# Performance work log

Measured on AMD Instinct MI355X. Metric: run time of the kernel, lower is better.

## Reference

```python
import jax, jax.numpy as jnp
import numpy as np

B, NV, NT = 256, 64, 77
UNIT_DIM, PROJ_DIM, V_HID, T_HID = 512, 512, 768, 512
TEMP_INIT = 0.07
LN_EPS = 1e-5
NORM_EPS = 1e-12


def _xavier(key, fan_in, fan_out):
    lim = np.sqrt(6.0 / (fan_in + fan_out))
    return jax.random.uniform(key, (fan_in, fan_out), jnp.float32, -lim, lim)


def _ln(x, g, b):
    mu = jnp.mean(x, axis=-1, keepdims=True)
    var = jnp.mean(jnp.square(x - mu), axis=-1, keepdims=True)
    return (x - mu) * jax.lax.rsqrt(var + LN_EPS) * g + b


def _l2norm(x):
    n = jnp.sqrt(jnp.sum(jnp.square(x), axis=-1, keepdims=True))
    return x / jnp.maximum(n, NORM_EPS)


def _unit_mlp(x, W1, b1, g, bt, W2, b2):
    # Linear -> LayerNorm -> GELU(exact) -> Linear
    h = x @ W1 + b1
    h = jax.nn.gelu(_ln(h, g, bt), approximate=False)
    return h @ W2 + b2


def setup_inputs() -> dict:
    key = jax.random.key(0)
    ks = jax.random.split(key, 12)
    inp = {
        'visual_units': jax.random.normal(ks[0], (B, NV, UNIT_DIM), jnp.float32),
        'text_units': jax.random.normal(ks[1], (B, NT, UNIT_DIM), jnp.float32),
        'visual_cls': jax.random.normal(ks[2], (B, V_HID), jnp.float32),
        'text_cls': jax.random.normal(ks[3], (B, T_HID), jnp.float32),
        # visual unit proj
        'vW1': _xavier(ks[4], UNIT_DIM, PROJ_DIM), 'vb1': jnp.zeros(PROJ_DIM),
        'vg': jnp.ones(PROJ_DIM), 'vbt': jnp.zeros(PROJ_DIM),
        'vW2': _xavier(ks[5], PROJ_DIM, PROJ_DIM), 'vb2': jnp.zeros(PROJ_DIM),
        # text unit proj
        'tW1': _xavier(ks[6], UNIT_DIM, PROJ_DIM), 'tb1': jnp.zeros(PROJ_DIM),
        'tg': jnp.ones(PROJ_DIM), 'tbt': jnp.zeros(PROJ_DIM),
        'tW2': _xavier(ks[7], PROJ_DIM, PROJ_DIM), 'tb2': jnp.zeros(PROJ_DIM),
        # global projections (Linear -> LayerNorm)
        'gvW': _xavier(ks[8], V_HID, PROJ_DIM), 'gvb': jnp.zeros(PROJ_DIM),
        'gvg': jnp.ones(PROJ_DIM), 'gvbt': jnp.zeros(PROJ_DIM),
        'gtW': _xavier(ks[9], T_HID, PROJ_DIM), 'gtb': jnp.zeros(PROJ_DIM),
        'gtg': jnp.ones(PROJ_DIM), 'gtbt': jnp.zeros(PROJ_DIM),
        'logit_scale': jnp.log(jnp.asarray(1.0 / TEMP_INIT, jnp.float32)),
    }
    return inp


def _forward(visual_units, text_units, visual_cls, text_cls,
             vW1, vb1, vg, vbt, vW2, vb2,
             tW1, tb1, tg, tbt, tW2, tb2,
             gvW, gvb, gvg, gvbt, gtW, gtb, gtg, gtbt, logit_scale):
    # unit projections, L2-normalized: [B,Nv,P], [B,Nt,P]
    v_proj = _l2norm(_unit_mlp(visual_units, vW1, vb1, vg, vbt, vW2, vb2))
    t_proj = _l2norm(_unit_mlp(text_units, tW1, tb1, tg, tbt, tW2, tb2))
    # global projections, L2-normalized: [B,P]
    v_global = _l2norm(_ln(visual_cls @ gvW + gvb, gvg, gvbt))
    t_global = _l2norm(_ln(text_cls @ gtW + gtb, gtg, gtbt))

    scale = jnp.minimum(jnp.exp(logit_scale), 100.0)

    # ---- global CLIP loss ----
    logits = scale * (v_global @ t_global.T)  # [B,B]
    diag = jnp.arange(B)
    lp_i2t = jax.nn.log_softmax(logits, axis=-1)
    lp_t2i = jax.nn.log_softmax(logits.T, axis=-1)
    loss_global = -(jnp.mean(lp_i2t[diag, diag]) + jnp.mean(lp_t2i[diag, diag])) / 2.0

    # ---- unit-level mutual-NN loss (vectorized version of the python loop) ----
    sim = jnp.einsum('bvp,btp->bvt', v_proj, t_proj) * scale  # [B,Nv,Nt]
    logp_i2t = jax.nn.log_softmax(sim, axis=-1)   # over Nt
    logp_t2i = jax.nn.log_softmax(sim, axis=-2)   # over Nv
    best_t_for_v = jnp.argmax(sim, axis=-1)       # [B,Nv]
    best_v_for_t = jnp.argmax(sim, axis=-2)       # [B,Nt]
    # mutual mask: best_v_for_t[b, best_t_for_v[b,i]] == i
    back = jnp.take_along_axis(best_v_for_t, best_t_for_v, axis=1)  # [B,Nv]
    mutual = (back == jnp.arange(NV)[None, :])                      # [B,Nv] bool
    j = best_t_for_v[..., None]                                     # [B,Nv,1]
    lp1 = jnp.take_along_axis(logp_i2t, j, axis=2)[..., 0]          # [B,Nv]
    lp2 = jnp.take_along_axis(logp_t2i, j, axis=2)[..., 0]          # [B,Nv]
    m = mutual.astype(sim.dtype)
    loss_sum = -jnp.sum(m * (lp1 + lp2))
    count = 2.0 * jnp.sum(m)  # always >= 2B: the per-sample argmax of sim is mutual
    loss_unit = loss_sum / jnp.maximum(count, 1.0)

    # ---- diversity loss ----
    def _diversity(units, n):
        u = _l2norm(units)
        s = jnp.einsum('bip,bjp->bij', u, u)
        mask = 1.0 - jnp.eye(n, dtype=s.dtype)
        return jnp.sum(jnp.abs(s) * mask) / (B * n * (n - 1))
    loss_div = (_diversity(visual_units, NV) + _diversity(text_units, NT)) / 2.0

    sim_matrix = jnp.einsum('bvp,btp->bvt', v_proj, t_proj)
    return loss_global, loss_unit, loss_div, v_proj, t_proj, v_global, t_global, sim_matrix


def reference(visual_units, text_units, visual_cls, text_cls,
              vW1, vb1, vg, vbt, vW2, vb2,
              tW1, tb1, tg, tbt, tW2, tb2,
              gvW, gvb, gvg, gvbt, gtW, gtb, gtg, gtbt, logit_scale):
    return _forward(visual_units, text_units, visual_cls, text_cls,
                    vW1, vb1, vg, vbt, vW2, vb2,
                    tW1, tb1, tg, tbt, tW2, tb2,
                    gvW, gvb, gvg, gvbt, gtW, gtb, gtg, gtbt, logit_scale)
```

## Files before the change

### kernel.cpp

```cpp
#include <hip/hip_runtime.h>
#include <math.h>

typedef __attribute__((ext_vector_type(8))) short short8;
typedef __attribute__((ext_vector_type(4))) short short4v;
typedef __attribute__((ext_vector_type(4))) float f32x4;

#define NB 256
#define NVU 64
#define NTU 77
#define PD 512

#define O_VP 3ull
#define O_TP (O_VP + (size_t)NB * NVU * PD)
#define O_VG (O_TP + (size_t)NB * NTU * PD)
#define O_TG (O_VG + (size_t)NB * PD)
#define O_SM (O_TG + (size_t)NB * PD)

#define WS_VW1T 0u
#define WS_VW2T 524288u
#define WS_TW1T 1048576u
#define WS_TW2T 1572864u
#define WS_GVWT 2097152u
#define WS_GTWT 2883584u
#define WS_LOG  3552256u
#define WS_DIAG 3814400u
#define WS_RLSE 3815424u
#define WS_CLSE 3816448u
#define WS_UP   3817472u
#define WS_UC   3818496u
#define WS_PART 3819520u

#define GL_LDS16(gp, lp) __builtin_amdgcn_global_load_lds( \
    (const __attribute__((address_space(1))) void*)(gp), \
    (__attribute__((address_space(3))) void*)(lp), 16, 0, 0)

__device__ inline short f2bf(float f) {
  union { float f; unsigned u; } v; v.f = f;
  unsigned r = v.u + 0x7FFFu + ((v.u >> 16) & 1u);
  return (short)(r >> 16);
}
__device__ inline float bf2f(short s) {
  union { unsigned u; float f; } v; v.u = ((unsigned)(unsigned short)s) << 16;
  return v.f;
}

__device__ inline float blk_sum_(float x, float* buf, int nw) {
  const int lane = threadIdx.x & 63, w = threadIdx.x >> 6;
  #pragma unroll
  for (int m = 1; m < 64; m <<= 1) x += __shfl_xor(x, m, 64);
  __syncthreads();
  if (lane == 0) buf[w] = x;
  __syncthreads();
  float s = 0.f;
  for (int i = 0; i < nw; ++i) s += buf[i];
  return s;
}
__device__ inline float blk_max_(float x, float* buf, int nw) {
  const int lane = threadIdx.x & 63, w = threadIdx.x >> 6;
  #pragma unroll
  for (int m = 1; m < 64; m <<= 1) x = fmaxf(x, __shfl_xor(x, m, 64));
  __syncthreads();
  if (lane == 0) buf[w] = x;
  __syncthreads();
  float s = buf[0];
  for (int i = 1; i < nw; ++i) s = fmaxf(s, buf[i]);
  return s;
}

__global__ __launch_bounds__(256) void k_cvt_frag4(
    const float* __restrict__ s0, const float* __restrict__ s1,
    const float* __restrict__ s2, const float* __restrict__ s3,
    short* __restrict__ d0, short* __restrict__ d1,
    short* __restrict__ d2, short* __restrict__ d3) {
  int m = blockIdx.x >> 10;
  const float* src = m == 0 ? s0 : m == 1 ? s1 : m == 2 ? s2 : s3;
  short* dst = m == 0 ? d0 : m == 1 ? d1 : m == 2 ? d2 : d3;
  int idx = (blockIdx.x & 1023) * 256 + threadIdx.x;
  int k = idx >> 9, n = idx & 511;
  int kc = k >> 5, t = k & 31;
  int s = t >> 3, j = t & 7;
  int sw = (s ^ ((n >> 1) & 3)) << 3;
  dst[(size_t)kc * 16384 + n * 32 + sw + j] = f2bf(src[idx]);
}

__global__ __launch_bounds__(256) void k_transpose2(
    const float* __restrict__ gv, short* __restrict__ dv_,
    const float* __restrict__ gt, short* __restrict__ dt_) {
  int bid = blockIdx.x;
  if (bid < 1536) {
    int idx = bid * 256 + threadIdx.x;
    int k = idx >> 9, n = idx & 511;
    dv_[(size_t)n * 768 + k] = f2bf(gv[idx]);
  } else {
    int idx = (bid - 1536) * 256 + threadIdx.x;
    int k = idx >> 9, n = idx & 511;
    dt_[(size_t)n * 512 + k] = f2bf(gt[idx]);
  }
}

__global__ __launch_bounds__(1024) void k_unit_mlp11(
    const float* __restrict__ Xv, const float* __restrict__ Xt,
    const short* __restrict__ vWf1, const float* __restrict__ vb1,
    const float* __restrict__ vg, const float* __restrict__ vbt,
    const short* __restrict__ vWf2, const float* __restrict__ vb2,
    const short* __restrict__ tWf1, const float* __restrict__ tb1,
    const float* __restrict__ tg, const float* __restrict__ tbt,
    const short* __restrict__ tWf2, const float* __restrict__ tb2,
    float* __restrict__ outV, float* __restrict__ outT) {
  __shared__ __align__(16) short As[64][520];
  __shared__ __align__(16) short Bs[2][16384];
  __shared__ float redS[4][64];
  __shared__ float redQ[4][64];

  const int tid = threadIdx.x;
  const int w = tid >> 6, lane = tid & 63;
  const int rg = w >> 2, cg = w & 3;
  const int hi = lane >> 4, lo = lane & 15;

  const int xcd = blockIdx.x & 7, ii = blockIdx.x >> 3;
  const int orig = (xcd < 4 ? xcd * 71 : 284 + (xcd - 4) * 70) + ii;
  const bool isv = orig < 256;
  const int rb = isv ? orig : orig - 256;
  const float* __restrict__ X   = isv ? Xv : Xt;
  const short* __restrict__ Wf1 = isv ? vWf1 : tWf1;
  const float* __restrict__ b1  = isv ? vb1  : tb1;
  const float* __restrict__ gg  = isv ? vg   : tg;
  const float* __restrict__ bt  = isv ? vbt  : tbt;
  const short* __restrict__ Wf2 = isv ? vWf2 : tWf2;
  const float* __restrict__ b2  = isv ? vb2  : tb2;
  float* __restrict__ outF      = isv ? outV : outT;
  const size_t row0 = (size_t)rb * 64;

  const int arow = rg * 16 + lo;
  const int bswz = (cg * 128 + lo) * 32 + ((hi ^ ((lo >> 1) & 3)) * 8);

  GL_LDS16(Wf1 + tid * 8, &Bs[0][tid * 8]);
  GL_LDS16(Wf1 + 8192 + tid * 8, &Bs[0][8192 + tid * 8]);

  const f32x4* Xp = (const f32x4*)(X + row0 * 512);
  #pragma unroll
  for (int i = 0; i < 8; ++i) {
    int idx = i * 1024 + tid;
    f32x4 f = __builtin_nontemporal_load(Xp + idx);
    short4v s4 = {f2bf(f[0]), f2bf(f[1]), f2bf(f[2]), f2bf(f[3])};
    *(short4v*)&As[idx >> 7][(idx & 127) * 4] = s4;
  }
  __syncthreads();

  f32x4 acc[8];
  #pragma unroll
  for (int ct = 0; ct < 8; ++ct) acc[ct] = (f32x4){0.f, 0.f, 0.f, 0.f};

  GL_LDS16(Wf1 + 16384 + tid * 8, &Bs[1][tid * 8]);
  GL_LDS16(Wf1 + 16384 + 8192 + tid * 8, &Bs[1][8192 + tid * 8]);

  for (int kc = 0; kc < 16; ++kc) {
    const int cur = kc & 1;
    short8 a = *(const short8*)&As[arow][kc * 32 + hi * 8];
    #pragma unroll
    for (int ct = 0; ct < 8; ++ct) {
      short8 bb = *(const short8*)&Bs[cur][bswz + ct * 512];
      acc[ct] = __builtin_amdgcn_mfma_f32_16x16x32_bf16(a, bb, acc[ct], 0, 0, 0);
    }
    __builtin_amdgcn_s_barrier();
    const int nc = kc + 2;
    const short* nxt = (nc < 16) ? (Wf1 + (size_t)nc * 16384)
                                 : (Wf2 + (size_t)(nc - 16) * 16384);
    GL_LDS16(nxt + tid * 8, &Bs[cur][tid * 8]);
    GL_LDS16(nxt + 8192 + tid * 8, &Bs[cur][8192 + tid * 8]);
    asm volatile("s_waitcnt vmcnt(2)" ::: "memory");
  }

  {
    float ps[4] = {0.f, 0.f, 0.f, 0.f}, pq[4] = {0.f, 0.f, 0.f, 0.f};
    #pragma unroll
    for (int ct = 0; ct < 8; ++ct) {
      float bia = b1[cg * 128 + ct * 16 + lo];
      #pragma unroll
      for (int r = 0; r < 4; ++r) {
        float v = acc[ct][r] + bia;
        acc[ct][r] = v;
        ps[r] += v; pq[r] += v * v;
      }
    }
    #pragma unroll
    for (int m = 1; m < 16; m <<= 1)
      #pragma unroll
      for (int r = 0; r < 4; ++r) {
        ps[r] += __shfl_xor(ps[r], m, 64);
        pq[r] += __shfl_xor(pq[r], m, 64);
      }
    if (lo == 0) {
      #pragma unroll
      for (int r = 0; r < 4; ++r) {
        int rr = rg * 16 + hi * 4 + r;
        redS[cg][rr] = ps[r]; redQ[cg][rr] = pq[r];
      }
    }
  }
  __syncthreads();

  {
    float mu[4], rs[4];
    #pragma unroll
    for (int r = 0; r < 4; ++r) {
      int rr = rg * 16 + hi * 4 + r;
      float s = redS[0][rr] + redS[1][rr] + redS[2][rr] + redS[3][rr];
      float q = redQ[0][rr] + redQ[1][rr] + redQ[2][rr] + redQ[3][rr];
      float m_ = s * (1.f / 512.f);
      mu[r] = m_;
      rs[r] = rsqrtf(q * (1.f / 512.f) - m_ * m_ + 1e-5f);
    }
    #pragma unroll
    for (int ct = 0; ct < 8; ++ct) {
      int col = cg * 128 + ct * 16 + lo;
      float ga = gg[col], be = bt[col];
      #pragma unroll
      for (int r = 0; r < 4; ++r) {
        float xn = (acc[ct][r] - mu[r]) * rs[r] * ga + be;
        float ge = 0.5f * xn * (1.f + erff(xn * 0.70710678118654752f));
        As[rg * 16 + hi * 4 + r][col] = f2bf(ge);
      }
    }
  }
  __syncthreads();

  #pragma unroll
  for (int ct = 0; ct < 8; ++ct) acc[ct] = (f32x4){0.f, 0.f, 0.f, 0.f};
  for (int kc = 0; kc < 16; ++kc) {
    const int cur = kc & 1;
    short8 a = *(const short8*)&As[arow][kc * 32 + hi * 8];
    #pragma unroll
    for (int ct = 0; ct < 8; ++ct) {
      short8 bb = *(const short8*)&Bs[cur][bswz + ct * 512];
      acc[ct] = __builtin_amdgcn_mfma_f32_16x16x32_bf16(a, bb, acc[ct], 0, 0, 0);
    }
    __builtin_amdgcn_s_barrier();
    if (kc < 14) {
      const short* nxt = Wf2 + (size_t)(kc + 2) * 16384;
      GL_LDS16(nxt + tid * 8, &Bs[cur][tid * 8]);
      GL_LDS16(nxt + 8192 + tid * 8, &Bs[cur][8192 + tid * 8]);
      asm volatile("s_waitcnt vmcnt(2)" ::: "memory");
    } else if (kc == 14) {
      asm volatile("s_waitcnt vmcnt(0)" ::: "memory");
    }
  }

  {
    float pq[4] = {0.f, 0.f, 0.f, 0.f};
    #pragma unroll
    for (int ct = 0; ct < 8; ++ct) {
      float bia = b2[cg * 128 + ct * 16 + lo];
      #pragma unroll
      for (int r = 0; r < 4; ++r) {
        float v = acc[ct][r] + bia;
        acc[ct][r] = v;
        pq[r] += v * v;
      }
    }
    #pragma unroll
    for (int m = 1; m < 16; m <<= 1)
      #pragma unroll
      for (int r = 0; r < 4; ++r) pq[r] += __shfl_xor(pq[r], m, 64);
    if (lo == 0) {
      #pragma unroll
      for (int r = 0; r < 4; ++r) redQ[cg][rg * 16 + hi * 4 + r] = pq[r];
    }
  }
  __syncthreads();
  {
    float invn[4];
    #pragma unroll
    for (int r = 0; r < 4; ++r) {
      int rr = rg * 16 + hi * 4 + r;
      float q = redQ[0][rr] + redQ[1][rr] + redQ[2][rr] + redQ[3][rr];
      invn[r] = 1.f / fmaxf(sqrtf(q), 1e-12f);
    }
    #pragma unroll
    for (int ct = 0; ct < 8; ++ct) {
      int col = cg * 128 + ct * 16 + lo;
      #pragma unroll
      for (int r = 0; r < 4; ++r)
        outF[(row0 + rg * 16 + hi * 4 + r) * 512 + col] = acc[ct][r] * invn[r];
    }
  }
}

__global__ __launch_bounds__(256) void k_gproj2(
    const float* __restrict__ vsrc, const float* __restrict__ tsrc,
    const short* __restrict__ vWT, const float* __restrict__ vbias,
    const float* __restrict__ vgg, const float* __restrict__ vbt,
    const short* __restrict__ tWT, const float* __restrict__ tbias,
    const float* __restrict__ tgg, const float* __restrict__ tbt,
    float* __restrict__ outV, float* __restrict__ outT) {
  __shared__ float srow[768];
  __shared__ float rbuf[4];
  const bool isv = blockIdx.x < 256;
  const int row = blockIdx.x & 255, tid = threadIdx.x;
  const int K = isv ? 768 : 512;
  const float* src = isv ? vsrc : tsrc;
  const short* WT = isv ? vWT : tWT;
  const float* bias = isv ? vbias : tbias;
  const float* gg = isv ? vgg : tgg;
  const float* bt = isv ? vbt : tbt;
  float* outp = isv ? outV : outT;

  for (int k = tid; k < K; k += 256) srow[k] = src[(size_t)row * K + k];
  __syncthreads();
  float v0 = 0.f, v1 = 0.f;
  const short* wp0 = WT + (size_t)tid * K;
  const short* wp1 = WT + (size_t)(tid + 256) * K;
  for (int k = 0; k < K; k += 8) {
    short8 wa = *(const short8*)(wp0 + k);
    short8 wb = *(const short8*)(wp1 + k);
    #pragma unroll
    for (int j = 0; j < 8; ++j) {
      float sv = srow[k + j];
      v0 += sv * bf2f(wa[j]);
      v1 += sv * bf2f(wb[j]);
    }
  }
  v0 += bias[tid]; v1 += bias[tid + 256];
  float s = blk_sum_(v0 + v1, rbuf, 4);
  float q = blk_sum_(v0 * v0 + v1 * v1, rbuf, 4);
  float mu = s * (1.f / 512.f);
  float var = q * (1.f / 512.f) - mu * mu;
  float rs = rsqrtf(var + 1e-5f);
  float y0 = (v0 - mu) * rs * gg[tid] + bt[tid];
  float y1 = (v1 - mu) * rs * gg[tid + 256] + bt[tid + 256];
  float ss = blk_sum_(y0 * y0 + y1 * y1, rbuf, 4);
  float invn = 1.f / fmaxf(sqrtf(ss), 1e-12f);
  outp[(size_t)row * 512 + tid] = y0 * invn;
  outp[(size_t)row * 512 + tid + 256] = y1 * invn;
}

__global__ __launch_bounds__(256) void k_logits_row(
    const float* __restrict__ vgp, const float* __restrict__ tgp,
    const float* __restrict__ lsc, float* __restrict__ logits,
    float* __restrict__ diag, float* __restrict__ rlse) {
  __shared__ __align__(16) float vrow[512];
  __shared__ float rbuf[4];
  const int i = blockIdx.x, tid = threadIdx.x;
  const float scale = fminf(expf(lsc[0]), 100.f);
  vrow[tid] = vgp[(size_t)i * 512 + tid];
  vrow[tid + 256] = vgp[(size_t)i * 512 + 256 + tid];
  __syncthreads();
  const float4* tp4 = (const float4*)(tgp + (size_t)tid * 512);
  const float4* v4 = (const float4*)vrow;
  float s = 0.f;
  for (int k = 0; k < 128; ++k) {
    float4 t = tp4[k], vv = v4[k];
    s += t.x * vv.x + t.y * vv.y + t.z * vv.z + t.w * vv.w;
  }
  float lg = scale * s;
  logits[(size_t)i * 256 + tid] = lg;
  if (tid == i) diag[i] = lg;
  float mx = blk_max_(lg, rbuf, 4);
  float se = blk_sum_(expf(lg - mx), rbuf, 4);
  if (tid == 0) rlse[i] = mx + logf(se);
}

__global__ __launch_bounds__(256) void k_logits_col(
    const float* __restrict__ logits, float* __restrict__ clse) {
  __shared__ float rbuf[4];
  const int j = blockIdx.x, tid = threadIdx.x;
  float lg = logits[(size_t)tid * 256 + j];
  float mx = blk_max_(lg, rbuf, 4);
  float se = blk_sum_(expf(lg - mx), rbuf, 4);
  if (tid == 0) clse[j] = mx + logf(se);
}

__global__ __launch_bounds__(512) void k_unit_sim(
    const float* __restrict__ vpp, const float* __restrict__ tpp,
    const float* __restrict__ lsc, float* __restrict__ simout,
    float* __restrict__ up, float* __restrict__ uc) {
  __shared__ float Sp[2][64][81];
  __shared__ float lse_r[64];
  __shared__ int bestt[64];
  __shared__ float lse_c[80];
  __shared__ int bestv[80];
  __shared__ float rbuf[8];
  const int b = blockIdx.x;
  const int tid = threadIdx.x;
  const int w = tid >> 6, lane = tid & 63;
  const int wq = w >> 1, kg = w & 1;
  const int hi = lane >> 4, lo = lane & 15;
  const float scale = fminf(expf(lsc[0]), 100.f);

  f32x4 acc[5];
  #pragma unroll
  for (int ct = 0; ct < 5; ++ct) acc[ct] = (f32x4){0.f, 0.f, 0.f, 0.f};

  const float* va = vpp + ((size_t)b * 64 + wq * 16 + lo) * 512 + kg * 256;
  const float* tbase = tpp + (size_t)b * 77 * 512 + kg * 256;
  for (int k0 = 0; k0 < 256; k0 += 32) {
    float4 f0 = *(const float4*)(va + k0 + hi * 8);
    float4 f1 = *(const float4*)(va + k0 + hi * 8 + 4);
    short8 a = {f2bf(f0.x), f2bf(f0.y), f2bf(f0.z), f2bf(f0.w),
                f2bf(f1.x), f2bf(f1.y), f2bf(f1.z), f2bf(f1.w)};
    #pragma unroll
    for (int ct = 0; ct < 5; ++ct) {
      int rj = ct * 16 + lo;
      short8 bb = {0, 0, 0, 0, 0, 0, 0, 0};
      if (rj < 77) {
        const float* tb = tbase + (size_t)rj * 512 + k0 + hi * 8;
        float4 g0 = *(const float4*)tb;
        float4 g1 = *(const float4*)(tb + 4);
        bb = (short8){f2bf(g0.x), f2bf(g0.y), f2bf(g0.z), f2bf(g0.w),
                      f2bf(g1.x), f2bf(g1.y), f2bf(g1.z), f2bf(g1.w)};
      }
      acc[ct] = __builtin_amdgcn_mfma_f32_16x16x32_bf16(a, bb, acc[ct], 0, 0, 0);
    }
  }
  #pragma unroll
  for (int ct = 0; ct < 5; ++ct)
    #pragma unroll
    for (int r = 0; r < 4; ++r) {
      int i = wq * 16 + hi * 4 + r, j = ct * 16 + lo;
      if (j < 77) Sp[kg][i][j] = acc[ct][r];
    }
  __syncthreads();
  for (int idx = tid; idx < 64 * 77; idx += 512) {
    int i = idx / 77, j = idx - i * 77;
    float s = Sp[0][i][j] + Sp[1][i][j];
    simout[((size_t)b * 64 + i) * 77 + j] = s;
    Sp[0][i][j] = s * scale;
  }
  __syncthreads();
  if (tid < 64) {
    float mx = -1e30f; int am = 0;
    for (int t = 0; t < 77; ++t) { float x = Sp[0][tid][t]; if (x > mx) { mx = x; am = t; } }
    float se = 0.f;
    for (int t = 0; t < 77; ++t) se += expf(Sp[0][tid][t] - mx);
    lse_r[tid] = mx + logf(se); bestt[tid] = am;
  } else if (tid < 64 + 77) {
    int t = tid - 64;
    float mx = -1e30f; int am = 0;
    for (int v = 0; v < 64; ++v) { float x = Sp[0][v][t]; if (x > mx) { mx = x; am = v; } }
    float se = 0.f;
    for (int v = 0; v < 64; ++v) se += expf(Sp[0][v][t] - mx);
    lse_c[t] = mx + logf(se); bestv[t] = am;
  }
  __syncthreads();
  float c = 0.f, cnt = 0.f;
  if (tid < 64) {
    int j = bestt[tid];
    if (bestv[j] == tid) {
      float sv = Sp[0][tid][j];
      c = -((sv - lse_r[tid]) + (sv - lse_c[j]));
      cnt = 2.f;
    }
  }
  c = blk_sum_(c, rbuf, 8);
  cnt = blk_sum_(cnt, rbuf, 8);
  if (tid == 0) { up[b] = c; uc[b] = cnt; }
}

__global__ __launch_bounds__(320) void k_div2(
    const float* __restrict__ Xv, const float* __restrict__ Xt,
    float* __restrict__ part) {
  __shared__ __align__(16) short Bsd[80][136];
  __shared__ float invs[80];
  __shared__ float rbuf[5];
  const int bid = blockIdx.x;
  const bool isv = bid < 256;
  const int b = bid & 255;
  const int N = isv ? 64 : 77;
  const float* X = (isv ? Xv : Xt) + (size_t)b * N * 512;
  const int w = threadIdx.x >> 6, lane = threadIdx.x & 63;
  const int hi = lane >> 4, lo = lane & 15;
  const int ri = w * 16 + lo;

  f32x4 acc[5];
  #pragma unroll
  for (int ct = 0; ct < 5; ++ct) acc[ct] = (f32x4){0.f, 0.f, 0.f, 0.f};

  for (int c = 0; c < 4; ++c) {
    for (int s = threadIdx.x; s < 80 * 32; s += 320) {
      int r = s >> 5, cgp = s & 31;
      short4v s4 = {0, 0, 0, 0};
      if (r < N) {
        float4 f = *(const float4*)(X + (size_t)r * 512 + c * 128 + cgp * 4);
        s4 = (short4v){f2bf(f.x), f2bf(f.y), f2bf(f.z), f2bf(f.w)};
      }
      *(short4v*)&Bsd[r][cgp * 4] = s4;
    }
    __syncthreads();
    #pragma unroll
    for (int kc = 0; kc < 4; ++kc) {
      short8 a = *(const short8*)&Bsd[ri][kc * 32 + hi * 8];
      #pragma unroll
      for (int ct = 0; ct < 5; ++ct) {
        short8 bb = *(const short8*)&Bsd[ct * 16 + lo][kc * 32 + hi * 8];
        acc[ct] = __builtin_amdgcn_mfma_f32_16x16x32_bf16(a, bb, acc[ct], 0, 0, 0);
      }
    }
    __syncthreads();
  }

  #pragma unroll
  for (int ct = 0; ct < 5; ++ct)
    #pragma unroll
    for (int r = 0; r < 4; ++r) {
      int i = w * 16 + hi * 4 + r, j = ct * 16 + lo;
      if (i == j && i < N) invs[i] = 1.f / fmaxf(sqrtf(fmaxf(acc[ct][r], 0.f)), 1e-12f);
    }
  __syncthreads();

  float cs = 0.f;
  #pragma unroll
  for (int ct = 0; ct < 5; ++ct)
    #pragma unroll
    for (int r = 0; r < 4; ++r) {
      int i = w * 16 + hi * 4 + r, j = ct * 16 + lo;
      if (i < N && j < N && i != j)
        cs += fabsf(acc[ct][r]) * invs[i] * invs[j];
    }
  #pragma unroll
  for (int m = 1; m < 64; m <<= 1) cs += __shfl_xor(cs, m, 64);
  if (lane == 0) rbuf[w] = cs;
  __syncthreads();
  if (threadIdx.x == 0) {
    float s = 0.f;
    for (int i = 0; i < 5; ++i) s += rbuf[i];
    part[bid] = s;
  }
}

__global__ __launch_bounds__(256) void k_final(
    const float* __restrict__ diag, const float* __restrict__ rlse,
    const float* __restrict__ clse, const float* __restrict__ up,
    const float* __restrict__ uc, const float* __restrict__ part,
    float* __restrict__ out) {
  __shared__ float rbuf[4];
  const int tid = threadIdx.x;
  float d = diag[tid];
  float s1 = blk_sum_(d - rlse[tid], rbuf, 4);
  float s2 = blk_sum_(d - clse[tid], rbuf, 4);
  float su = blk_sum_(up[tid], rbuf, 4);
  float sc = blk_sum_(uc[tid], rbuf, 4);
  float sv = blk_sum_(part[tid], rbuf, 4);
  float st = blk_sum_(part[tid + 256], rbuf, 4);
  if (tid == 0) {
    out[0] = -(s1 * (1.f / 256.f) + s2 * (1.f / 256.f)) * 0.5f;
    out[1] = su / fmaxf(sc, 1.f);
    out[2] = (sv / (256.f * 64.f * 63.f) + st / (256.f * 77.f * 76.f)) * 0.5f;
  }
}

extern "C" void kernel_launch(void* const* d_in, const int* in_sizes, int n_in,
                              void* d_out, int out_size, void* d_ws, size_t ws_size,
                              hipStream_t stream) {
  const float* vis_units = (const float*)d_in[0];
  const float* txt_units = (const float*)d_in[1];
  const float* vis_cls = (const float*)d_in[2];
  const float* txt_cls = (const float*)d_in[3];
  const float* vW1 = (const float*)d_in[4];
  const float* vb1 = (const float*)d_in[5];
  const float* vg  = (const float*)d_in[6];
  const float* vbt = (const float*)d_in[7];
  const float* vW2 = (const float*)d_in[8];
  const float* vb2 = (const float*)d_in[9];
  const float* tW1 = (const float*)d_in[10];
  const float* tb1 = (const float*)d_in[11];
  const float* tg  = (const float*)d_in[12];
  const float* tbt = (const float*)d_in[13];
  const float* tW2 = (const float*)d_in[14];
  const float* tb2 = (const float*)d_in[15];
  const float* gvW = (const float*)d_in[16];
  const float* gvb = (const float*)d_in[17];
  const float* gvg = (const float*)d_in[18];
  const float* gvbt = (const float*)d_in[19];
  const float* gtW = (const float*)d_in[20];
  const float* gtb = (const float*)d_in[21];
  const float* gtg = (const float*)d_in[22];
  const float* gtbt = (const float*)d_in[23];
  const float* lsc = (const float*)d_in[24];

  float* out = (float*)d_out;
  char* ws = (char*)d_ws;
  short* vW1T = (short*)(ws + WS_VW1T);
  short* vW2T = (short*)(ws + WS_VW2T);
  short* tW1T = (short*)(ws + WS_TW1T);
  short* tW2T = (short*)(ws + WS_TW2T);
  short* gvWT = (short*)(ws + WS_GVWT);
  short* gtWT = (short*)(ws + WS_GTWT);
  float* logits = (float*)(ws + WS_LOG);
  float* diag = (float*)(ws + WS_DIAG);
  float* rlse = (float*)(ws + WS_RLSE);
  float* clse = (float*)(ws + WS_CLSE);
  float* up = (float*)(ws + WS_UP);
  float* uc = (float*)(ws + WS_UC);
  float* part = (float*)(ws + WS_PART);

  k_cvt_frag4<<<4096, 256, 0, stream>>>(vW1, vW2, tW1, tW2, vW1T, vW2T, tW1T, tW2T);
  k_transpose2<<<2560, 256, 0, stream>>>(gvW, gvWT, gtW, gtWT);

  k_unit_mlp11<<<564, 1024, 0, stream>>>(
      vis_units, txt_units,
      vW1T, vb1, vg, vbt, vW2T, vb2,
      tW1T, tb1, tg, tbt, tW2T, tb2,
      out + O_VP, out + O_TP);

  k_gproj2<<<512, 256, 0, stream>>>(vis_cls, txt_cls,
      gvWT, gvb, gvg, gvbt, gtWT, gtb, gtg, gtbt,
      out + O_VG, out + O_TG);

  k_logits_row<<<256, 256, 0, stream>>>(out + O_VG, out + O_TG, lsc, logits, diag, rlse);
  k_logits_col<<<256, 256, 0, stream>>>(logits, clse);

  k_unit_sim<<<256, 512, 0, stream>>>(out + O_VP, out + O_TP, lsc, out + O_SM, up, uc);

  k_div2<<<512, 320, 0, stream>>>(vis_units, txt_units, part);

  k_final<<<1, 256, 0, stream>>>(diag, rlse, clse, up, uc, part, out);

  (void)in_sizes; (void)n_in; (void)out_size; (void)ws_size;
}
```

Before: 257.9 us.

## Coalesce weight conversion and logits access via transposed layouts

The weight-conversion kernel now stages a 32x64 tile in shared memory and writes 16-byte vectors into the swizzled fragment layout, replacing scattered 2-byte stores. The global text projection is also written transposed to a workspace buffer so the row-logits kernel reads it coalesced across threads. A transposed copy of the logits is written so the column log-sum-exp reads contiguously. In exchange there are extra uncoalesced scattered writes in gproj and logits_row, plus more workspace.

```diff
diff --git a/kernel.cpp b/kernel.cpp
--- a/kernel.cpp
+++ b/kernel.cpp
@@ -29,6 +29,8 @@
 #define WS_UP   3817472u
 #define WS_UC   3818496u
 #define WS_PART 3819520u
+#define WS_TT   3821568u
+#define WS_LOGT 4345856u
 
 #define GL_LDS16(gp, lp) __builtin_amdgcn_global_load_lds( \
     (const __attribute__((address_space(1))) void*)(gp), \
@@ -67,20 +69,31 @@
   return s;
 }
 
-__global__ __launch_bounds__(256) void k_cvt_frag4(
+__global__ __launch_bounds__(256) void k_cvt_frag4b(
     const float* __restrict__ s0, const float* __restrict__ s1,
     const float* __restrict__ s2, const float* __restrict__ s3,
     short* __restrict__ d0, short* __restrict__ d1,
     short* __restrict__ d2, short* __restrict__ d3) {
-  int m = blockIdx.x >> 10;
+  __shared__ short tile[32][66];
+  const int m = blockIdx.x >> 7;
   const float* src = m == 0 ? s0 : m == 1 ? s1 : m == 2 ? s2 : s3;
   short* dst = m == 0 ? d0 : m == 1 ? d1 : m == 2 ? d2 : d3;
-  int idx = (blockIdx.x & 1023) * 256 + threadIdx.x;
-  int k = idx >> 9, n = idx & 511;
-  int kc = k >> 5, t = k & 31;
-  int s = t >> 3, j = t & 7;
-  int sw = (s ^ ((n >> 1) & 3)) << 3;
-  dst[(size_t)kc * 16384 + n * 32 + sw + j] = f2bf(src[idx]);
+  const int rem = blockIdx.x & 127;
+  const int kc = rem >> 3, nt = rem & 7;
+  const int n0 = nt * 64;
+  #pragma unroll
+  for (int it = 0; it < 8; ++it) {
+    int idx = it * 256 + threadIdx.x;
+    int r = idx >> 6, c = idx & 63;
+    tile[r][c] = f2bf(src[(size_t)(kc * 32 + r) * 512 + n0 + c]);
+  }
+  __syncthreads();
+  const int nl = threadIdx.x >> 2, s = threadIdx.x & 3;
+  const int n = n0 + nl;
+  short8 v;
+  #pragma unroll
+  for (int j = 0; j < 8; ++j) v[j] = tile[s * 8 + j][nl];
+  *(short8*)&dst[(size_t)kc * 16384 + n * 32 + ((s ^ ((n >> 1) & 3)) << 3)] = v;
 }
 
 __global__ __launch_bounds__(256) void k_transpose2(
@@ -292,7 +305,8 @@
     const float* __restrict__ vgg, const float* __restrict__ vbt,
     const short* __restrict__ tWT, const float* __restrict__ tbias,
     const float* __restrict__ tgg, const float* __restrict__ tbt,
-    float* __restrict__ outV, float* __restrict__ outT) {
+    float* __restrict__ outV, float* __restrict__ outT,
+    float* __restrict__ Tt) {
   __shared__ float srow[768];
   __shared__ float rbuf[4];
   const bool isv = blockIdx.x < 256;
@@ -330,13 +344,19 @@
   float y1 = (v1 - mu) * rs * gg[tid + 256] + bt[tid + 256];
   float ss = blk_sum_(y0 * y0 + y1 * y1, rbuf, 4);
   float invn = 1.f / fmaxf(sqrtf(ss), 1e-12f);
-  outp[(size_t)row * 512 + tid] = y0 * invn;
-  outp[(size_t)row * 512 + tid + 256] = y1 * invn;
+  float o0 = y0 * invn, o1 = y1 * invn;
+  outp[(size_t)row * 512 + tid] = o0;
+  outp[(size_t)row * 512 + tid + 256] = o1;
+  if (!isv) {
+    Tt[(size_t)tid * 256 + row] = o0;
+    Tt[(size_t)(tid + 256) * 256 + row] = o1;
+  }
 }
 
 __global__ __launch_bounds__(256) void k_logits_row(
-    const float* __restrict__ vgp, const float* __restrict__ tgp,
+    const float* __restrict__ vgp, const float* __restrict__ Tt,
     const float* __restrict__ lsc, float* __restrict__ logits,
+    float* __restrict__ logitsT,
     float* __restrict__ diag, float* __restrict__ rlse) {
   __shared__ __align__(16) float vrow[512];
   __shared__ float rbuf[4];
@@ -345,15 +365,13 @@
   vrow[tid] = vgp[(size_t)i * 512 + tid];
   vrow[tid + 256] = vgp[(size_t)i * 512 + 256 + tid];
   __syncthreads();
-  const float4* tp4 = (const float4*)(tgp + (size_t)tid * 512);
-  const float4* v4 = (const float4*)vrow;
   float s = 0.f;
-  for (int k = 0; k < 128; ++k) {
-    float4 t = tp4[k], vv = v4[k];
-    s += t.x * vv.x + t.y * vv.y + t.z * vv.z + t.w * vv.w;
-  }
+  #pragma unroll 8
+  for (int k = 0; k < 512; ++k)
+    s += vrow[k] * Tt[(size_t)k * 256 + tid];
   float lg = scale * s;
   logits[(size_t)i * 256 + tid] = lg;
+  logitsT[(size_t)tid * 256 + i] = lg;
   if (tid == i) diag[i] = lg;
   float mx = blk_max_(lg, rbuf, 4);
   float se = blk_sum_(expf(lg - mx), rbuf, 4);
@@ -361,10 +379,10 @@
 }
 
 __global__ __launch_bounds__(256) void k_logits_col(
-    const float* __restrict__ logits, float* __restrict__ clse) {
+    const float* __restrict__ logitsT, float* __restrict__ clse) {
   __shared__ float rbuf[4];
   const int j = blockIdx.x, tid = threadIdx.x;
-  float lg = logits[(size_t)tid * 256 + j];
+  float lg = logitsT[(size_t)j * 256 + tid];
   float mx = blk_max_(lg, rbuf, 4);
   float se = blk_sum_(expf(lg - mx), rbuf, 4);
   if (tid == 0) clse[j] = mx + logf(se);
@@ -592,8 +610,10 @@
   float* up = (float*)(ws + WS_UP);
   float* uc = (float*)(ws + WS_UC);
   float* part = (float*)(ws + WS_PART);
-
-  k_cvt_frag4<<<4096, 256, 0, stream>>>(vW1, vW2, tW1, tW2, vW1T, vW2T, tW1T, tW2T);
+  float* Tt = (float*)(ws + WS_TT);
+  float* logitsT = (float*)(ws + WS_LOGT);
+
+  k_cvt_frag4b<<<512, 256, 0, stream>>>(vW1, vW2, tW1, tW2, vW1T, vW2T, tW1T, tW2T);
   k_transpose2<<<2560, 256, 0, stream>>>(gvW, gvWT, gtW, gtWT);
 
   k_unit_mlp11<<<564, 1024, 0, stream>>>(
@@ -604,10 +624,10 @@
 
   k_gproj2<<<512, 256, 0, stream>>>(vis_cls, txt_cls,
       gvWT, gvb, gvg, gvbt, gtWT, gtb, gtg, gtbt,
-      out + O_VG, out + O_TG);
-
-  k_logits_row<<<256, 256, 0, stream>>>(out + O_VG, out + O_TG, lsc, logits, diag, rlse);
-  k_logits_col<<<256, 256, 0, stream>>>(logits, clse);
+      out + O_VG, out + O_TG, Tt);
+
+  k_logits_row<<<256, 256, 0, stream>>>(out + O_VG, Tt, lsc, logits, logitsT, diag, rlse);
+  k_logits_col<<<256, 256, 0, stream>>>(logitsT, clse);
 
   k_unit_sim<<<256, 512, 0, stream>>>(out + O_VP, out + O_TP, lsc, out + O_SM, up, uc);
 
```

After: 262.6 us. No clear change (+1.8%).
